# Performance work log

Measured on AMD Instinct MI355X. Metric: run time of the kernel, lower is better.

## Reference

```python
import jax, jax.numpy as jnp
import numpy as np

HEADS = 8
DIM_HEAD = 64
SCALE = DIM_HEAD ** -0.5


def setup_inputs() -> dict:
    key = jax.random.key(0)
    ks = jax.random.split(key, 5)
    dim, hidden = 512, HEADS * DIM_HEAD
    b, l = 4, 2048
    return {
        "x": jax.random.normal(ks[0], (b, dim, l), jnp.float32),
        "w_qkv": jax.random.normal(ks[1], (3 * hidden, dim), jnp.float32) * 0.02,
        "b_qkv": jax.random.normal(ks[2], (3 * hidden,), jnp.float32) * 0.02,
        "w_out": jax.random.normal(ks[3], (dim, hidden), jnp.float32) * 0.02,
        "b_out": jax.random.normal(ks[4], (dim,), jnp.float32) * 0.02,
    }


def reference(x, w_qkv, b_qkv, w_out, b_out):
    b, c, l = x.shape
    # Conv1d kernel-size-1 == per-position linear: (b, 3*hidden, l)
    qkv = jnp.einsum('oc,bcl->bol', w_qkv, x) + b_qkv[None, :, None]
    q, k, v = jnp.split(qkv, 3, axis=1)
    # rearrange 'b (h d) l -> b h d l'
    def split_heads(t):
        return t.reshape(b, HEADS, DIM_HEAD, l)
    q, k, v = split_heads(q) * SCALE, split_heads(k), split_heads(v)
    sim = jnp.einsum('bhdi,bhdj->bhij', q, k)  # [b,h,l,l]
    sim = sim - jax.lax.stop_gradient(jnp.max(sim, axis=-1, keepdims=True))
    attn = jax.nn.softmax(sim, axis=-1)
    out = jnp.einsum('bhij,bhdj->bhid', attn, v)  # [b,h,l,d]
    # 'b h l d -> b (h d) l'
    out = out.transpose(0, 1, 3, 2).reshape(b, HEADS * DIM_HEAD, l)
    out = jnp.einsum('oc,bcl->bol', w_out, out) + b_out[None, :, None]
    return out
```

## Files before the change

### kernel.cpp

```cpp
#include <hip/hip_runtime.h>
#include <hip/hip_bf16.h>

#define B 4
#define DIM 512
#define HID 512
#define NH 8
#define DH 64
#define L 2048
#define QSCALE (0.125f * 1.4426950408889634f)

typedef __attribute__((ext_vector_type(8)))  short bf16x8;
typedef __attribute__((ext_vector_type(4)))  float f32x4;
typedef __attribute__((ext_vector_type(16))) float f32x16;
typedef __attribute__((ext_vector_type(4)))  int   i32x4;

static __device__ __forceinline__ short f32_to_bf16s(float f) {
    __hip_bfloat16 h = __float2bfloat16(f);
    return *reinterpret_cast<short*>(&h);
}
static __device__ __forceinline__ float bf16s_to_f32(short s) {
    return __uint_as_float(((unsigned)(unsigned short)s) << 16);
}

static __device__ __forceinline__ float fast_exp2(float x) {
    float r;
    asm("v_exp_f32 %0, %1" : "=v"(r) : "v"(x));
    return r;
}

static __device__ __forceinline__ void gl_lds16(const short* g, short* l) {
    __builtin_amdgcn_global_load_lds(
        (const __attribute__((address_space(1))) void*)g,
        (__attribute__((address_space(3))) void*)l, 16, 0, 0);
}

static __device__ __forceinline__ bf16x8 lds_frag(const short* t, int row, int c) {
    bf16x8 v;
    __builtin_memcpy(&v, t + row * 64 + ((c ^ (row & 7)) * 8), 16);
    return v;
}

__global__ __launch_bounds__(256) void prep(
    const float* __restrict__ wq, const float* __restrict__ wo,
    short* __restrict__ wdst,
    const float* __restrict__ X, short* __restrict__ XT)
{
    const int bx  = blockIdx.x;
    const int tid = threadIdx.x;
    if (bx < 1024) {
        const int i = (bx * 256 + tid) * 4;
        float4 v;
        if (i < 786432) v = *(const float4*)(wq + i);
        else            v = *(const float4*)(wo + (i - 786432));
        short4 pk = {f32_to_bf16s(v.x), f32_to_bf16s(v.y),
                     f32_to_bf16s(v.z), f32_to_bf16s(v.w)};
        *(short4*)(wdst + i) = pk;
        return;
    }
    const int bid = bx - 1024;
    const int l0 = (bid & 31) * 64;
    const int c0 = ((bid >> 5) & 7) * 64;
    const int b  = bid >> 8;

    __shared__ float tile[64][65];
    const float* Xb = X + (size_t)b * DIM * L;

    #pragma unroll
    for (int it = 0; it < 16; ++it) {
        const int cr = (tid >> 6) + it * 4;
        const int lc = tid & 63;
        tile[cr][lc] = Xb[(size_t)(c0 + cr) * L + l0 + lc];
    }
    __syncthreads();
    short* XTb = XT + (size_t)b * L * DIM;
    #pragma unroll
    for (int it = 0; it < 8; ++it) {
        const int l  = (tid >> 5) + it * 8;
        const int c2 = (tid & 31) * 2;
        short2 pk = {f32_to_bf16s(tile[c2][l]), f32_to_bf16s(tile[c2 + 1][l])};
        *(short2*)(XTb + (size_t)(l0 + l) * DIM + c0 + c2) = pk;
    }
}

__global__ __launch_bounds__(256) void qkv_mfma(
    const short* __restrict__ Wb, const short* __restrict__ XT,
    const float* __restrict__ bias,
    short* __restrict__ qws, short* __restrict__ kws, short* __restrict__ vws)
{
    const int lBase = blockIdx.x * 128;
    const int oBase = blockIdx.y * 128;
    const int b     = blockIdx.z;
    const int tid   = threadIdx.x;
    const int wave  = tid >> 6;
    const int lane  = tid & 63;
    const int lid   = lane & 15;
    const int quad  = lane >> 4;
    const int rsub  = lane >> 3;
    const int cl    = (lane & 7) ^ rsub;

    __shared__ __align__(16) short Wt[128 * 64];
    __shared__ __align__(16) short Xt[128 * 64];

    const short* XTb = XT + (size_t)b * L * DIM;
    const int oLoc = (wave & 1) * 64;
    const int lLoc = (wave >> 1) * 64;

    f32x4 acc[4][4];
    #pragma unroll
    for (int mi = 0; mi < 4; ++mi)
        #pragma unroll
        for (int ni = 0; ni < 4; ++ni) acc[mi][ni] = (f32x4){0.f, 0.f, 0.f, 0.f};

    for (int c0 = 0; c0 < DIM; c0 += 64) {
        if (c0) __syncthreads();
        #pragma unroll
        for (int t = 0; t < 4; ++t) {
            const int ch = wave * 4 + t;
            const int r  = ch * 8 + rsub;
            gl_lds16(Wb  + (size_t)(oBase + r) * DIM + c0 + cl * 8, Wt + ch * 512);
            gl_lds16(XTb + (size_t)(lBase + r) * DIM + c0 + cl * 8, Xt + ch * 512);
        }
        __syncthreads();
        #pragma unroll
        for (int kc = 0; kc < 2; ++kc) {
            bf16x8 a[4], bb[4];
            #pragma unroll
            for (int mi = 0; mi < 4; ++mi)
                a[mi] = lds_frag(Wt, oLoc + mi * 16 + lid, kc * 4 + quad);
            #pragma unroll
            for (int ni = 0; ni < 4; ++ni)
                bb[ni] = lds_frag(Xt, lLoc + ni * 16 + lid, kc * 4 + quad);
            #pragma unroll
            for (int mi = 0; mi < 4; ++mi)
                #pragma unroll
                for (int ni = 0; ni < 4; ++ni)
                    acc[mi][ni] = __builtin_amdgcn_mfma_f32_16x16x32_bf16(
                        a[mi], bb[ni], acc[mi][ni], 0, 0, 0);
        }
    }

    const int rty = oBase >> 9;
    const float sc = (rty == 0) ? QSCALE : 1.0f;
    const int h = ((oBase + oLoc) >> 6) & 7;
    const int pl = (lid & 3) | ((lid & 4) << 1) | ((lid & 8) >> 1);

    #pragma unroll
    for (int mi = 0; mi < 4; ++mi) {
        const int dB = mi * 16 + quad * 4;
        float bia[4];
        #pragma unroll
        for (int r = 0; r < 4; ++r)
            bia[r] = bias[oBase + oLoc + mi * 16 + quad * 4 + r];

        if (rty < 2) {
            short* dst = (rty == 0 ? qws : kws) + (((size_t)b * NH + h) * L) * DH;
            #pragma unroll
            for (int ni = 0; ni < 4; ++ni) {
                const int l = lBase + lLoc + ni * 16 + lid;
                short4 pk = {f32_to_bf16s((acc[mi][ni][0] + bia[0]) * sc),
                             f32_to_bf16s((acc[mi][ni][1] + bia[1]) * sc),
                             f32_to_bf16s((acc[mi][ni][2] + bia[2]) * sc),
                             f32_to_bf16s((acc[mi][ni][3] + bia[3]) * sc)};
                *(short4*)(dst + (size_t)l * DH + dB) = pk;
            }
        } else {
            short* dst = vws + (((size_t)b * NH + h) * DH) * L;
            #pragma unroll
            for (int r = 0; r < 4; ++r) {
                const int d = dB + r;
                #pragma unroll
                for (int ni = 0; ni < 4; ++ni)
                    dst[(size_t)d * L + lBase + lLoc + ni * 16 + pl] =
                        f32_to_bf16s((acc[mi][ni][r] + bia[r]) * sc);
            }
        }
    }
}

__global__ __launch_bounds__(256) void attn_mfma(
    const short* __restrict__ Q, const short* __restrict__ K,
    const short* __restrict__ VT,
    short* __restrict__ Op0, short* __restrict__ Op1,
    short* __restrict__ Op2, short* __restrict__ Op3,
    float* __restrict__ Lp)
{
    const int h     = blockIdx.x >> 2;
    const int qtr   = blockIdx.x & 3;
    const int b     = blockIdx.y;
    const int iTile = blockIdx.z;
    const int tid   = threadIdx.x;
    const int wave  = tid >> 6;
    const int lane  = tid & 63;
    const int l5    = lane & 31;
    const int me    = lane >> 5;
    const int rsub  = lane >> 3;
    const int cl    = (lane & 7) ^ rsub;

    short* __restrict__ Op = (qtr & 2) ? ((qtr & 1) ? Op3 : Op2)
                                       : ((qtr & 1) ? Op1 : Op0);
    float* __restrict__ Lq = Lp + (size_t)qtr * (B * NH * L);

    const size_t headOff = ((size_t)b * NH + h) * (size_t)L * DH;
    const short* Qh = Q + headOff;
    const short* Kh = K + headOff;
    const short* Vh = VT + headOff;

    __shared__ __align__(16) short Kt[64 * 64];
    __shared__ __align__(16) short Vt[64 * 64];

    const int q0 = iTile * 128 + wave * 32;
    bf16x8 qf[4];
    #pragma unroll
    for (int kc = 0; kc < 4; ++kc)
        qf[kc] = *(const bf16x8*)(Qh + (size_t)(q0 + l5) * DH + kc * 16 + me * 8);

    f32x16 oacc[2];
    #pragma unroll
    for (int dt = 0; dt < 2; ++dt)
        #pragma unroll
        for (int r = 0; r < 16; ++r) oacc[dt][r] = 0.f;
    float lsum = 0.f;

    const int jt0 = qtr * 8;
    for (int it = 0; it < 8; ++it) {
        const int j0 = (jt0 + it) * 64;
        if (it) __syncthreads();
        #pragma unroll
        for (int t = 0; t < 2; ++t) {
            const int ch = wave * 2 + t;
            const int r  = ch * 8 + rsub;
            gl_lds16(Kh + (size_t)(j0 + r) * DH + cl * 8, Kt + ch * 512);
            gl_lds16(Vh + (size_t)r * L + j0 + cl * 8,    Vt + ch * 512);
        }
        __syncthreads();

        unsigned dw[2][4][2];
        #pragma unroll
        for (int mt = 0; mt < 2; ++mt) {
            f32x16 s;
            #pragma unroll
            for (int r = 0; r < 16; ++r) s[r] = 0.f;
            #pragma unroll
            for (int kc = 0; kc < 4; ++kc) {
                bf16x8 a = lds_frag(Kt, mt * 32 + l5, kc * 2 + me);
                s = __builtin_amdgcn_mfma_f32_32x32x16_bf16(a, qf[kc], s, 0, 0, 0);
            }
            #pragma unroll
            for (int g = 0; g < 4; ++g) {
                #pragma unroll
                for (int p = 0; p < 2; ++p) {
                    const float p0 = fast_exp2(s[4 * g + 2 * p]);
                    const float p1 = fast_exp2(s[4 * g + 2 * p + 1]);
                    const unsigned pk = __builtin_amdgcn_perm(
                        __float_as_uint(p1), __float_as_uint(p0), 0x07060302u);
                    lsum += __uint_as_float(pk << 16);
                    lsum += __uint_as_float(pk & 0xffff0000u);
                    dw[mt][g][p] = pk;
                }
            }
        }

        #pragma unroll
        for (int mt = 0; mt < 2; ++mt) {
            #pragma unroll
            for (int kl = 0; kl < 2; ++kl) {
                i32x4 bi = {(int)dw[mt][2 * kl][0], (int)dw[mt][2 * kl][1],
                            (int)dw[mt][2 * kl + 1][0], (int)dw[mt][2 * kl + 1][1]};
                bf16x8 pb = __builtin_bit_cast(bf16x8, bi);
                const int ch = (mt * 2 + kl) * 2 + me;
                #pragma unroll
                for (int dt = 0; dt < 2; ++dt) {
                    bf16x8 a = lds_frag(Vt, dt * 32 + l5, ch);
                    oacc[dt] = __builtin_amdgcn_mfma_f32_32x32x16_bf16(a, pb, oacc[dt], 0, 0, 0);
                }
            }
        }
    }

    const float vh = lsum + __shfl_xor(lsum, 32);
    const int qg = q0 + l5;
    if (me == 0)
        Lq[((size_t)b * NH + h) * L + qg] = vh;

    const float inv = 1.0f / vh;
    short* ab = Op + ((size_t)b * L + qg) * HID + h * DH;
    #pragma unroll
    for (int dt = 0; dt < 2; ++dt) {
        #pragma unroll
        for (int g = 0; g < 4; ++g) {
            const int d = dt * 32 + 8 * g + me * 4;
            short4 pk = {f32_to_bf16s(oacc[dt][4 * g]     * inv),
                         f32_to_bf16s(oacc[dt][4 * g + 1] * inv),
                         f32_to_bf16s(oacc[dt][4 * g + 2] * inv),
                         f32_to_bf16s(oacc[dt][4 * g + 3] * inv)};
            *(short4*)(ab + d) = pk;
        }
    }
}

__global__ __launch_bounds__(256) void combine4(
    const short* __restrict__ O0, const short* __restrict__ O1,
    const short* __restrict__ O2, const short* __restrict__ O3,
    const float* __restrict__ Lp, short* __restrict__ Abf)
{
    const int g = blockIdx.x * 256 + threadIdx.x;
    const int i = g * 4;
    const int b = i >> 20;
    const int rem = i & 1048575;
    const int l = rem >> 9;
    const int c = rem & 511;
    const int h = c >> 6;
    const size_t li = ((size_t)b * NH + h) * L + l;
    const float w0 = Lp[li];
    const float w1 = Lp[li + (size_t)B * NH * L];
    const float w2 = Lp[li + (size_t)2 * B * NH * L];
    const float w3 = Lp[li + (size_t)3 * B * NH * L];
    const float inv = 1.0f / (w0 + w1 + w2 + w3);
    const short4 a = *(const short4*)(O0 + i);
    const short4 bb = *(const short4*)(O1 + i);
    const short4 cc = *(const short4*)(O2 + i);
    const short4 dd = *(const short4*)(O3 + i);
    short4 pk = {
        f32_to_bf16s((w0 * bf16s_to_f32(a.x) + w1 * bf16s_to_f32(bb.x) +
                      w2 * bf16s_to_f32(cc.x) + w3 * bf16s_to_f32(dd.x)) * inv),
        f32_to_bf16s((w0 * bf16s_to_f32(a.y) + w1 * bf16s_to_f32(bb.y) +
                      w2 * bf16s_to_f32(cc.y) + w3 * bf16s_to_f32(dd.y)) * inv),
        f32_to_bf16s((w0 * bf16s_to_f32(a.z) + w1 * bf16s_to_f32(bb.z) +
                      w2 * bf16s_to_f32(cc.z) + w3 * bf16s_to_f32(dd.z)) * inv),
        f32_to_bf16s((w0 * bf16s_to_f32(a.w) + w1 * bf16s_to_f32(bb.w) +
                      w2 * bf16s_to_f32(cc.w) + w3 * bf16s_to_f32(dd.w)) * inv)};
    *(short4*)(Abf + i) = pk;
}

__global__ __launch_bounds__(256) void out_mfma(
    const short* __restrict__ Wo, const short* __restrict__ Abf,
    const float* __restrict__ bias, float* __restrict__ out)
{
    const int lBase = blockIdx.x * 128;
    const int oBase = blockIdx.y * 64;
    const int b     = blockIdx.z;
    const int tid   = threadIdx.x;
    const int wave  = tid >> 6;
    const int lane  = tid & 63;
    const int lid   = lane & 15;
    const int quad  = lane >> 4;
    const int rsub  = lane >> 3;
    const int cl    = (lane & 7) ^ rsub;

    __shared__ __align__(16) short Wt[64 * 64];
    __shared__ __align__(16) short At[128 * 64];

    const short* Ab = Abf + (size_t)b * L * HID;
    const int oLoc = (wave & 1) * 32;
    const int lLoc = (wave >> 1) * 64;

    f32x4 acc[2][4];
    #pragma unroll
    for (int mi = 0; mi < 2; ++mi)
        #pragma unroll
        for (int ni = 0; ni < 4; ++ni) acc[mi][ni] = (f32x4){0.f, 0.f, 0.f, 0.f};

    for (int c0 = 0; c0 < HID; c0 += 64) {
        if (c0) __syncthreads();
        #pragma unroll
        for (int t = 0; t < 2; ++t) {
            const int ch = wave * 2 + t;
            const int r  = ch * 8 + rsub;
            gl_lds16(Wo + (size_t)(oBase + r) * HID + c0 + cl * 8, Wt + ch * 512);
        }
        #pragma unroll
        for (int t = 0; t < 4; ++t) {
            const int ch = wave * 4 + t;
            const int r  = ch * 8 + rsub;
            gl_lds16(Ab + (size_t)(lBase + r) * HID + c0 + cl * 8, At + ch * 512);
        }
        __syncthreads();
        #pragma unroll
        for (int kc = 0; kc < 2; ++kc) {
            bf16x8 a[2], bb[4];
            #pragma unroll
            for (int mi = 0; mi < 2; ++mi)
                a[mi] = lds_frag(Wt, oLoc + mi * 16 + lid, kc * 4 + quad);
            #pragma unroll
            for (int ni = 0; ni < 4; ++ni)
                bb[ni] = lds_frag(At, lLoc + ni * 16 + lid, kc * 4 + quad);
            #pragma unroll
            for (int mi = 0; mi < 2; ++mi)
                #pragma unroll
                for (int ni = 0; ni < 4; ++ni)
                    acc[mi][ni] = __builtin_amdgcn_mfma_f32_16x16x32_bf16(
                        a[mi], bb[ni], acc[mi][ni], 0, 0, 0);
        }
    }

    #pragma unroll
    for (int mi = 0; mi < 2; ++mi) {
        #pragma unroll
        for (int r = 0; r < 4; ++r) {
            const int o = oBase + oLoc + mi * 16 + quad * 4 + r;
            const float bia = bias[o];
            #pragma unroll
            for (int ni = 0; ni < 4; ++ni)
                out[((size_t)b * DIM + o) * L + lBase + lLoc + ni * 16 + lid] =
                    acc[mi][ni][r] + bia;
        }
    }
}

extern "C" void kernel_launch(void* const* d_in, const int* in_sizes, int n_in,
                              void* d_out, int out_size, void* d_ws, size_t ws_size,
                              hipStream_t stream)
{
    const float* x     = (const float*)d_in[0];
    const float* w_qkv = (const float*)d_in[1];
    const float* b_qkv = (const float*)d_in[2];
    const float* w_out = (const float*)d_in[3];
    const float* b_out = (const float*)d_in[4];
    float* out = (float*)d_out;

    char* w = (char*)d_ws;
    short* xT  = (short*)(w);
    short* wqb = (short*)(w + (8u << 20));
    short* wob = wqb + 786432;
    short* qws = (short*)(w + (10u << 20));
    short* kws = (short*)(w + (18u << 20));
    short* vws = (short*)(w + (26u << 20));
    short* Abf = (short*)(w + (34u << 20));
    short* Op1 = (short*)(w);
    short* Op2 = (short*)(w + (42u << 20));
    short* Op3 = (short*)(w + (50u << 20));
    float* Lp  = (float*)(w + (58u << 20));
    short* Op0 = (short*)d_out;

    dim3 blk(256);
    prep<<<dim3(2048), blk, 0, stream>>>(w_qkv, w_out, wqb, x, xT);
    qkv_mfma<<<dim3(L / 128, 1536 / 128, B), blk, 0, stream>>>(
        wqb, xT, b_qkv, qws, kws, vws);
    attn_mfma<<<dim3(NH * 4, B, L / 128), blk, 0, stream>>>(
        qws, kws, vws, Op0, Op1, Op2, Op3, Lp);
    combine4<<<dim3(4096), blk, 0, stream>>>(Op0, Op1, Op2, Op3, Lp, Abf);
    out_mfma<<<dim3(L / 128, DIM / 64, B), blk, 0, stream>>>(
        wob, Abf, b_out, out);
}
```

Baseline: 161.9 us.

## Double-buffer K/V LDS tiles to overlap the next tile's load with compute

Each of the K and V shared-memory tiles becomes two buffers. The first tile is preloaded before the loop, and each iteration issues the async global-to-LDS loads for the next tile into the other buffer before running the QK and PV MFMAs on the current one. This hides global load latency behind the matrix work and drops to one barrier per iteration. In exchange, LDS use per block doubles, which may lower occupancy, and only eight iterations are available to amortise the prologue.

```diff
diff --git a/kernel.cpp b/kernel.cpp
--- a/kernel.cpp
+++ b/kernel.cpp
@@ -205,8 +205,8 @@
     const short* Kh = K + headOff;
     const short* Vh = VT + headOff;
 
-    __shared__ __align__(16) short Kt[64 * 64];
-    __shared__ __align__(16) short Vt[64 * 64];
+    __shared__ __align__(16) short Kt[2 * 4096];
+    __shared__ __align__(16) short Vt[2 * 4096];
 
     const int q0 = iTile * 128 + wave * 32;
     bf16x8 qf[4];
@@ -222,17 +222,31 @@
     float lsum = 0.f;
 
     const int jt0 = qtr * 8;
+    const int ch0 = wave * 2;
+    const int r0  = ch0 * 8 + rsub;
+    const int r1  = r0 + 8;
+
+    {
+        const int j0 = jt0 * 64;
+        gl_lds16(Kh + (size_t)(j0 + r0) * DH + cl * 8, Kt + ch0 * 512);
+        gl_lds16(Vh + (size_t)r0 * L + j0 + cl * 8,    Vt + ch0 * 512);
+        gl_lds16(Kh + (size_t)(j0 + r1) * DH + cl * 8, Kt + ch0 * 512 + 512);
+        gl_lds16(Vh + (size_t)r1 * L + j0 + cl * 8,    Vt + ch0 * 512 + 512);
+    }
+
     for (int it = 0; it < 8; ++it) {
-        const int j0 = (jt0 + it) * 64;
-        if (it) __syncthreads();
-        #pragma unroll
-        for (int t = 0; t < 2; ++t) {
-            const int ch = wave * 2 + t;
-            const int r  = ch * 8 + rsub;
-            gl_lds16(Kh + (size_t)(j0 + r) * DH + cl * 8, Kt + ch * 512);
-            gl_lds16(Vh + (size_t)r * L + j0 + cl * 8,    Vt + ch * 512);
-        }
         __syncthreads();
+        if (it + 1 < 8) {
+            const int j0 = (jt0 + it + 1) * 64;
+            short* Kd = Kt + ((it + 1) & 1) * 4096 + ch0 * 512;
+            short* Vd = Vt + ((it + 1) & 1) * 4096 + ch0 * 512;
+            gl_lds16(Kh + (size_t)(j0 + r0) * DH + cl * 8, Kd);
+            gl_lds16(Vh + (size_t)r0 * L + j0 + cl * 8,    Vd);
+            gl_lds16(Kh + (size_t)(j0 + r1) * DH + cl * 8, Kd + 512);
+            gl_lds16(Vh + (size_t)r1 * L + j0 + cl * 8,    Vd + 512);
+        }
+        const short* Ktb = Kt + (it & 1) * 4096;
+        const short* Vtb = Vt + (it & 1) * 4096;
 
         unsigned dw[2][4][2];
         #pragma unroll
@@ -242,7 +256,7 @@
             for (int r = 0; r < 16; ++r) s[r] = 0.f;
             #pragma unroll
             for (int kc = 0; kc < 4; ++kc) {
-                bf16x8 a = lds_frag(Kt, mt * 32 + l5, kc * 2 + me);
+                bf16x8 a = lds_frag(Ktb, mt * 32 + l5, kc * 2 + me);
                 s = __builtin_amdgcn_mfma_f32_32x32x16_bf16(a, qf[kc], s, 0, 0, 0);
             }
             #pragma unroll
@@ -270,7 +284,7 @@
                 const int ch = (mt * 2 + kl) * 2 + me;
                 #pragma unroll
                 for (int dt = 0; dt < 2; ++dt) {
-                    bf16x8 a = lds_frag(Vt, dt * 32 + l5, ch);
+                    bf16x8 a = lds_frag(Vtb, dt * 32 + l5, ch);
                     oacc[dt] = __builtin_amdgcn_mfma_f32_32x32x16_bf16(a, pb, oacc[dt], 0, 0, 0);
                 }
             }
```

Result: slower. 169.0 us (+4.4%).
